# Kernel tuning notes

Hardware: AMD Instinct MI355X
Metric: run time of the kernel (lower is better)

## Reference

```python
import jax, jax.numpy as jnp
from jax import lax
import numpy as np

B, N, C = 8, 4096, 64
NPOINT = 1024
RADII = (0.1, 0.2, 0.4)
NSAMPLES = (16, 32, 128)
MLPS = ((32, 32, 64), (64, 64, 128), (64, 96, 128))


def setup_inputs() -> dict:
    key = jax.random.key(0)
    ks = jax.random.split(key, 32)
    inp = {
        "xyz": jax.random.uniform(ks[0], (B, N, 3), jnp.float32),
        "points": jax.random.normal(ks[1], (B, N, C), jnp.float32),
    }
    k = 2
    for bi, widths in enumerate(MLPS):
        cin = C + 3  # use_xyz concatenates relative coords
        for li, cout in enumerate(widths):
            inp[f"w{bi}_{li}"] = jax.random.normal(ks[k], (cin, cout), jnp.float32) * (1.0 / np.sqrt(cin))
            k += 1
            inp[f"b{bi}_{li}"] = jnp.zeros((cout,), jnp.float32)
            cin = cout
    return inp


def farthest_point_sample(xyz, npoint):
    # xyz: [B,N,3] -> idx [B,npoint] int32. Deterministic start at point 0.
    Bb, Nn, _ = xyz.shape

    def step(carry, _):
        dists, farthest = carry  # [B,N], [B]
        centroid = jnp.take_along_axis(xyz, farthest[:, None, None], axis=1)  # [B,1,3]
        d = jnp.sum((xyz - centroid) ** 2, axis=-1)
        dists = jnp.minimum(dists, d)
        return (dists, jnp.argmax(dists, axis=-1).astype(jnp.int32)), farthest

    init = (jnp.full((Bb, Nn), 1e10, xyz.dtype), jnp.zeros((Bb,), jnp.int32))
    _, idx = lax.scan(step, init, None, length=npoint)
    return jnp.transpose(idx)  # [B, npoint]


def _ball_query(d2, radius, nsample, Nn):
    # d2: [B,S,N] squared distances. First nsample indices (in original order)
    # within radius; empty slots filled with the first valid index (center
    # point is always within its own ball, so a valid index always exists).
    key = jnp.where(d2 < radius * radius, jnp.arange(Nn, dtype=jnp.int32), Nn)
    srt = jnp.sort(key, axis=-1)[..., :nsample]  # [B,S,nsample]
    first = srt[..., :1]
    return jnp.where(srt == Nn, first, srt)


def _group(x, idx):
    # x: [B,N,D], idx: [B,S,K] -> [B,S,K,D]
    return jax.vmap(lambda p, i: p[i])(x, idx)


def _forward(xyz, points, params):
    Nn = xyz.shape[1]
    fps_idx = farthest_point_sample(xyz, NPOINT)                 # [B,S]
    new_xyz = jnp.take_along_axis(xyz, fps_idx[..., None], axis=1)  # [B,S,3]
    d2 = jnp.sum((new_xyz[:, :, None, :] - xyz[:, None, :, :]) ** 2, axis=-1)  # [B,S,N]
    outs = []
    for r, ns, layers in zip(RADII, NSAMPLES, params):
        idx = _ball_query(d2, r, ns, Nn)                          # [B,S,ns]
        g_xyz = _group(xyz, idx) - new_xyz[:, :, None, :]         # [B,S,ns,3]
        g = jnp.concatenate([_group(points, idx), g_xyz], axis=-1)  # [B,S,ns,C+3]
        for w, b in layers:  # 1x1 Conv2d == per-neighbor dense + relu
            g = jax.nn.relu(g @ w + b)
        outs.append(jnp.max(g, axis=2))                           # [B,S,cout]
    return new_xyz, jnp.concatenate(outs, axis=-1)


def reference(xyz, points,
              w0_0, b0_0, w0_1, b0_1, w0_2, b0_2,
              w1_0, b1_0, w1_1, b1_1, w1_2, b1_2,
              w2_0, b2_0, w2_1, b2_1, w2_2, b2_2):
    params = [
        [(w0_0, b0_0), (w0_1, b0_1), (w0_2, b0_2)],
        [(w1_0, b1_0), (w1_1, b1_1), (w1_2, b1_2)],
        [(w2_0, b2_0), (w2_1, b2_1), (w2_2, b2_2)],
    ]
    return _forward(xyz, points, params)
```

## Files before the change

kernel.cpp:

```cpp
#include <hip/hip_runtime.h>
#include <hip/hip_bf16.h>
#include <stdint.h>

typedef unsigned long long u64;
typedef __attribute__((ext_vector_type(8))) short bf16x8;
typedef __attribute__((ext_vector_type(4))) float f32x4;
typedef __attribute__((ext_vector_type(2))) float f32x2;

#define SCOPE_AGENT __HIP_MEMORY_SCOPE_AGENT
#define POISON 0xFFFFFFFFu
#define SPIN_GUARD (1 << 22)

#define H_ITEM 0
#define H_PREP 1
#define H_PLACED 2
#define H_FDONE 3
#define H_SLEEP 4

__device__ __forceinline__ unsigned short f2bf(float f) {
    unsigned x = __float_as_uint(f);
    unsigned r = (x + 0x7fffu + ((x >> 16) & 1u)) >> 16;
    return (unsigned short)r;
}

__device__ __forceinline__ bf16x8 cvt8(float4 a, float4 b) {
    union { bf16x8 v; __hip_bfloat162 h[4]; } u;
    u.h[0] = __float22bfloat162_rn({a.x, a.y});
    u.h[1] = __float22bfloat162_rn({a.z, a.w});
    u.h[2] = __float22bfloat162_rn({b.x, b.y});
    u.h[3] = __float22bfloat162_rn({b.z, b.w});
    return u.v;
}

__device__ __forceinline__ float wave_max_dpp(float v) {
#define DPP_MAX_STEP(ctrl)                                                     \
    v = fmaxf(v, __int_as_float(__builtin_amdgcn_update_dpp(                   \
               0, __float_as_int(v), (ctrl), 0xf, 0xf, true)))
    DPP_MAX_STEP(0xB1);
    DPP_MAX_STEP(0x4E);
    DPP_MAX_STEP(0x141);
    DPP_MAX_STEP(0x140);
    DPP_MAX_STEP(0x142);
    DPP_MAX_STEP(0x143);
#undef DPP_MAX_STEP
    return __int_as_float(__builtin_amdgcn_readlane(__float_as_int(v), 63));
}

__device__ __forceinline__ void lds_barrier() {
    __builtin_amdgcn_sched_barrier(0);
    asm volatile("s_waitcnt lgkmcnt(0)" ::: "memory");
    __builtin_amdgcn_sched_barrier(0);
    __builtin_amdgcn_s_barrier();
    __builtin_amdgcn_sched_barrier(0);
}

__device__ __forceinline__ unsigned cu_key() {
    unsigned hw = (unsigned)__builtin_amdgcn_s_getreg(14852) & 0xffu;
    unsigned xcc = (unsigned)__builtin_amdgcn_s_getreg(6164) & 0x7u;
    return (xcc << 8) | hw;
}

struct WPack { const float* w[9]; const float* b[9]; };

__device__ __forceinline__ void fps_path(const float* __restrict__ xyz,
                                         float* __restrict__ newxyz,
                                         unsigned* __restrict__ hdr,
                                         unsigned* __restrict__ occ,
                                         unsigned char* smem) {
#pragma clang fp contract(off)
    __builtin_amdgcn_s_setprio(3);
    float* xs = (float*)smem;
    float* ys = xs + 4096;
    float* zs = ys + 4096;
    u64* skey = (u64*)(smem + 49152);

    const int b = blockIdx.x;
    const int t = threadIdx.x;
    const int lane = t & 63;
    const int wave = t >> 6;

    if (t == 0) {
        __hip_atomic_store(&occ[cu_key()], 1u, __ATOMIC_RELAXED, SCOPE_AGENT);
        __hip_atomic_fetch_add(&hdr[H_PLACED], 1u, __ATOMIC_RELEASE, SCOPE_AGENT);
    }

    f32x2 px[8], py[8], pz[8], dist[8];
    {
        union { float4 v[12]; float f[48]; } u;
        const float4* src =
            reinterpret_cast<const float4*>(xyz + (size_t)b * 12288) + t * 12;
#pragma unroll
        for (int w = 0; w < 12; ++w) u.v[w] = src[w];
#pragma unroll
        for (int i = 0; i < 8; ++i) {
            px[i] = (f32x2){u.f[6 * i + 0], u.f[6 * i + 3]};
            py[i] = (f32x2){u.f[6 * i + 1], u.f[6 * i + 4]};
            pz[i] = (f32x2){u.f[6 * i + 2], u.f[6 * i + 5]};
            dist[i] = (f32x2){1e10f, 1e10f};
            const int j = t * 16 + 2 * i;
            xs[j] = px[i].x; xs[j + 1] = px[i].y;
            ys[j] = py[i].x; ys[j + 1] = py[i].y;
            zs[j] = pz[i].x; zs[j + 1] = pz[i].y;
        }
    }
    __syncthreads();

    int far = 0;
    for (int k = 0; k < 1024; ++k) {
        const float cx = xs[far], cy = ys[far], cz = zs[far];
        if (t == 0) {
            const size_t o = ((size_t)b * 1024 + k) * 3;
            __hip_atomic_store(&newxyz[o + 0], cx, __ATOMIC_RELAXED, SCOPE_AGENT);
            __hip_atomic_store(&newxyz[o + 1], cy, __ATOMIC_RELAXED, SCOPE_AGENT);
            __hip_atomic_store(&newxyz[o + 2], cz, __ATOMIC_RELAXED, SCOPE_AGENT);
        }
        const f32x2 c2x = (f32x2){cx, cx};
        const f32x2 c2y = (f32x2){cy, cy};
        const f32x2 c2z = (f32x2){cz, cz};
#pragma unroll
        for (int i = 0; i < 8; ++i) {
            const f32x2 dx = px[i] - c2x;
            const f32x2 dy = py[i] - c2y;
            const f32x2 dz = pz[i] - c2z;
            const f32x2 s = dx * dx + dy * dy;
            const f32x2 d = s + dz * dz;
            dist[i].x = fminf(dist[i].x, d.x);
            dist[i].y = fminf(dist[i].y, d.y);
        }
        float dv[16];
#pragma unroll
        for (int i = 0; i < 8; ++i) { dv[2 * i] = dist[i].x; dv[2 * i + 1] = dist[i].y; }
        float m8[8], m4[4], bv;
#pragma unroll
        for (int i = 0; i < 8; ++i) m8[i] = fmaxf(dv[i], dv[i + 8]);
#pragma unroll
        for (int i = 0; i < 4; ++i) m4[i] = fmaxf(m8[i], m8[i + 4]);
        bv = fmaxf(fmaxf(m4[0], m4[1]), fmaxf(m4[2], m4[3]));
        int bj = 15;
#pragma unroll
        for (int i = 14; i >= 0; --i) bj = (dv[i] == bv) ? i : bj;
        const int myidx = t * 16 + bj;

        const float wmax = wave_max_dpp(bv);
        const u64 mask = __ballot(bv == wmax);
        const int fl = (int)__builtin_ctzll(mask);
        const int widx = __builtin_amdgcn_readlane(myidx, fl);

        const int pp = k & 1;
        if (lane == 0)
            skey[pp * 4 + wave] =
                ((u64)__float_as_uint(wmax) << 32) | (unsigned)(4095 - widx);
        lds_barrier();
        const ulonglong2 ka = *reinterpret_cast<const ulonglong2*>(&skey[pp * 4 + 0]);
        const ulonglong2 kb = *reinterpret_cast<const ulonglong2*>(&skey[pp * 4 + 2]);
        const u64 m01 = (ka.x > ka.y) ? ka.x : ka.y;
        const u64 m23 = (kb.x > kb.y) ? kb.x : kb.y;
        const u64 mm = (m01 > m23) ? m01 : m23;
        far = 4095 - (int)(unsigned)(mm & 0xffffffffull);
    }
    if (t == 0)
        __hip_atomic_fetch_add(&hdr[H_FDONE], 1u, __ATOMIC_RELEASE, SCOPE_AGENT);
}

__device__ __forceinline__ void prep_path(const WPack& p,
                                          unsigned short* __restrict__ wout,
                                          float* __restrict__ bout,
                                          unsigned* __restrict__ hdr) {
    constexpr int cin[9]  = {67, 32, 32,  67, 64, 64,  67, 64, 96};
    constexpr int cout[9] = {32, 32, 64,  64, 64, 128, 64, 96, 128};
    constexpr int sw[9]   = {104, 40, 40, 104, 72, 72, 104, 72, 104};
    constexpr int woff[9] = {0, 3328, 4608, 7168, 13824, 18432, 27648, 34304, 41216};
    constexpr int boff[9] = {0, 32, 64, 128, 192, 256, 384, 448, 544};
    const int L = blockIdx.x - 8;
    const float* w = p.w[L];
    const int ci = cin[L], co = cout[L], s = sw[L];
    unsigned short* dst = wout + woff[L];
    for (int e = threadIdx.x; e < co * s; e += 256) {
        const int n = e / s, k = e % s;
        dst[e] = (k < ci) ? f2bf(w[(size_t)k * co + n]) : (unsigned short)0;
    }
    for (int e = threadIdx.x; e < co; e += 256) bout[boff[L] + e] = p.b[L][e];
    __syncthreads();
    if (threadIdx.x == 0)
        __hip_atomic_fetch_add(&hdr[H_PREP], 1u, __ATOMIC_RELEASE, SCOPE_AGENT);
}

__device__ __forceinline__ void poll_centroid(const float* __restrict__ newxyz,
                                              int g, int lane,
                                              float& ncx, float& ncy, float& ncz) {
    const unsigned* ncw = (const unsigned*)(newxyz + (size_t)g * 3);
    unsigned w0 = 0, w1 = 0, w2 = 0;
    if (lane == 0) {
        int n = 0;
        for (;;) {
            w0 = __hip_atomic_load(&ncw[0], __ATOMIC_RELAXED, SCOPE_AGENT);
            w1 = __hip_atomic_load(&ncw[1], __ATOMIC_RELAXED, SCOPE_AGENT);
            w2 = __hip_atomic_load(&ncw[2], __ATOMIC_RELAXED, SCOPE_AGENT);
            if (w0 != POISON && w1 != POISON && w2 != POISON) break;
            if (++n > SPIN_GUARD) break;
            if (n < 64) __builtin_amdgcn_s_sleep(8);
            else        __builtin_amdgcn_s_sleep(32);
        }
    }
    ncx = __uint_as_float((unsigned)__builtin_amdgcn_readfirstlane((int)w0));
    ncy = __uint_as_float((unsigned)__builtin_amdgcn_readfirstlane((int)w1));
    ncz = __uint_as_float((unsigned)__builtin_amdgcn_readfirstlane((int)w2));
}

template <int NS>
__device__ __forceinline__ void ballq1(const float* __restrict__ base,
                                       float cx, float cy, float cz, float r2,
                                       unsigned short* __restrict__ out, int lane) {
    int cnt = 0, first = 0;
    const u64 lower = (((u64)1) << lane) - 1;
    for (int it = 0; it < 64; ++it) {
        const int j = it * 64 + lane;
        const float* pp = base + j * 3;
        const float dx = pp[0] - cx;
        const float dy = pp[1] - cy;
        const float dz = pp[2] - cz;
        const float d2 = __fadd_rn(__fadd_rn(__fmul_rn(dx, dx), __fmul_rn(dy, dy)),
                                   __fmul_rn(dz, dz));
        const bool in = d2 < r2;
        const u64 m = __ballot(in);
        if (cnt == 0 && m) first = it * 64 + (int)__builtin_ctzll(m);
        const int pos = cnt + (int)__builtin_popcountll(m & lower);
        if (in && pos < NS) out[pos] = (unsigned short)j;
        cnt += (int)__builtin_popcountll(m);
        if (cnt >= NS) break;
    }
    for (int pos = cnt + lane; pos < NS; pos += 64) out[pos] = (unsigned short)first;
}

template <int MW, int Cout, int SOUT>
__device__ __forceinline__ void layer1_direct(
    const float* __restrict__ pts,
    const float* __restrict__ xyzb,
    const unsigned short* __restrict__ idxb,
    float ncx, float ncy, float ncz,
    const unsigned short* __restrict__ Wg, const float* __restrict__ bg,
    unsigned short* __restrict__ dst, int lane, int mslice) {
    constexpr int SW = 104;
    constexpr int MT = MW / 16;
    constexpr int NT = Cout / 16;
    const int ml = lane & 15;
    const int quad = lane >> 4;

    bf16x8 afr[MT][3];
#pragma unroll
    for (int mt = 0; mt < MT; ++mt) {
        const int row = mslice * MW + mt * 16 + ml;
        const int id = idxb[row] & 4095;
        const float* rb = pts + ((size_t)id << 6) + quad * 8;
        const float4* r4 = reinterpret_cast<const float4*>(rb);
        afr[mt][0] = cvt8(r4[0], r4[1]);
        const float4* r4b = reinterpret_cast<const float4*>(rb + 32);
        afr[mt][1] = cvt8(r4b[0], r4b[1]);
        union { bf16x8 v; unsigned short h[8]; } tg;
        tg.v = (bf16x8)(short)0;
        if (quad == 0) {
            const float* pz = xyzb + (size_t)id * 3;
            tg.h[0] = f2bf(pz[0] - ncx);
            tg.h[1] = f2bf(pz[1] - ncy);
            tg.h[2] = f2bf(pz[2] - ncz);
        }
        afr[mt][2] = tg.v;
    }

    f32x4 acc[MT][NT];
#pragma unroll
    for (int mt = 0; mt < MT; ++mt)
#pragma unroll
        for (int nt = 0; nt < NT; ++nt) acc[mt][nt] = (f32x4){0.f, 0.f, 0.f, 0.f};

#pragma unroll
    for (int ks = 0; ks < 3; ++ks) {
        bf16x8 bfr[NT];
#pragma unroll
        for (int nt = 0; nt < NT; ++nt)
            bfr[nt] = *reinterpret_cast<const bf16x8*>(
                Wg + (nt * 16 + ml) * SW + ks * 32 + quad * 8);
#pragma unroll
        for (int mt = 0; mt < MT; ++mt)
#pragma unroll
            for (int nt = 0; nt < NT; ++nt)
                acc[mt][nt] = __builtin_amdgcn_mfma_f32_16x16x32_bf16(
                    afr[mt][ks], bfr[nt], acc[mt][nt], 0, 0, 0);
    }

#pragma unroll
    for (int nt = 0; nt < NT; ++nt) {
        const int col = nt * 16 + ml;
        const float bv = bg[col];
#pragma unroll
        for (int mt = 0; mt < MT; ++mt)
#pragma unroll
            for (int r = 0; r < 4; ++r) {
                const float v = fmaxf(acc[mt][nt][r] + bv, 0.0f);
                dst[(mslice * MW + mt * 16 + quad * 4 + r) * SOUT + col] = f2bf(v);
            }
    }
}

template <int MW, int Kp, int Cout, int SIN>
__device__ __forceinline__ void layer_mid(const unsigned short* __restrict__ src,
                                          unsigned short* __restrict__ dst,
                                          const unsigned short* __restrict__ Wg,
                                          const float* __restrict__ bg,
                                          int lane, int mslice) {
    constexpr int MT = MW / 16;
    constexpr int NT = Cout / 16;
    constexpr int SOUT = Cout + 8;
    const int ml = lane & 15;
    const int quad = lane >> 4;

    f32x4 acc[MT][NT];
#pragma unroll
    for (int mt = 0; mt < MT; ++mt)
#pragma unroll
        for (int nt = 0; nt < NT; ++nt) acc[mt][nt] = (f32x4){0.f, 0.f, 0.f, 0.f};

#pragma unroll
    for (int ks = 0; ks < Kp; ks += 32) {
        bf16x8 afr[MT], bfr[NT];
#pragma unroll
        for (int mt = 0; mt < MT; ++mt)
            afr[mt] = *reinterpret_cast<const bf16x8*>(
                src + (mslice * MW + mt * 16 + ml) * SIN + ks + quad * 8);
#pragma unroll
        for (int nt = 0; nt < NT; ++nt)
            bfr[nt] = *reinterpret_cast<const bf16x8*>(
                Wg + (nt * 16 + ml) * SIN + ks + quad * 8);
#pragma unroll
        for (int mt = 0; mt < MT; ++mt)
#pragma unroll
            for (int nt = 0; nt < NT; ++nt)
                acc[mt][nt] = __builtin_amdgcn_mfma_f32_16x16x32_bf16(
                    afr[mt], bfr[nt], acc[mt][nt], 0, 0, 0);
    }

#pragma unroll
    for (int nt = 0; nt < NT; ++nt) {
        const int col = nt * 16 + ml;
        const float bv = bg[col];
#pragma unroll
        for (int mt = 0; mt < MT; ++mt)
#pragma unroll
            for (int r = 0; r < 4; ++r) {
                const float v = fmaxf(acc[mt][nt][r] + bv, 0.0f);
                dst[(mslice * MW + mt * 16 + quad * 4 + r) * SOUT + col] = f2bf(v);
            }
    }
}

template <int MW, int Kp, int Cout, int SIN, bool DIRECT>
__device__ __forceinline__ void layer_last(const unsigned short* __restrict__ src,
                                           const unsigned short* __restrict__ Wg,
                                           const float* __restrict__ bg,
                                           float* __restrict__ out,
                                           int lane, int mslice) {
    constexpr int MT = MW / 16;
    constexpr int NT = Cout / 16;
    const int ml = lane & 15;
    const int quad = lane >> 4;

    f32x4 acc[MT][NT];
#pragma unroll
    for (int mt = 0; mt < MT; ++mt)
#pragma unroll
        for (int nt = 0; nt < NT; ++nt) acc[mt][nt] = (f32x4){0.f, 0.f, 0.f, 0.f};

#pragma unroll
    for (int ks = 0; ks < Kp; ks += 32) {
        bf16x8 afr[MT], bfr[NT];
#pragma unroll
        for (int mt = 0; mt < MT; ++mt)
            afr[mt] = *reinterpret_cast<const bf16x8*>(
                src + (mslice * MW + mt * 16 + ml) * SIN + ks + quad * 8);
#pragma unroll
        for (int nt = 0; nt < NT; ++nt)
            bfr[nt] = *reinterpret_cast<const bf16x8*>(
                Wg + (nt * 16 + ml) * SIN + ks + quad * 8);
#pragma unroll
        for (int mt = 0; mt < MT; ++mt)
#pragma unroll
            for (int nt = 0; nt < NT; ++nt)
                acc[mt][nt] = __builtin_amdgcn_mfma_f32_16x16x32_bf16(
                    afr[mt], bfr[nt], acc[mt][nt], 0, 0, 0);
    }

#pragma unroll
    for (int nt = 0; nt < NT; ++nt) {
        const int col = nt * 16 + ml;
        const float bv = bg[col];
        float mx = 0.0f;
#pragma unroll
        for (int mt = 0; mt < MT; ++mt)
#pragma unroll
            for (int r = 0; r < 4; ++r) mx = fmaxf(mx, acc[mt][nt][r] + bv);
        mx = fmaxf(mx, __shfl_xor(mx, 16, 64));
        mx = fmaxf(mx, __shfl_xor(mx, 32, 64));
        if (quad == 0) {
            if constexpr (DIRECT) out[col] = mx;
            else atomicMax(reinterpret_cast<int*>(out + col), __float_as_int(mx));
        }
    }
}

template <int NS, int C1, int C2, int C3, int CH_OFF>
__device__ __forceinline__ void consume_small(
    unsigned char* smem, const float* __restrict__ xyz,
    const float* __restrict__ points, const float* __restrict__ newxyz,
    const unsigned short* wg1, const unsigned short* wg2, const unsigned short* wg3,
    const float* bg1, const float* bg2, const float* bg3,
    float* __restrict__ outfeat, int gbase, int bb, float r2) {
    constexpr int SB = C1 + 8, SC = C2 + 8;
    unsigned short* Bb = (unsigned short*)smem;
    unsigned short* Cb = Bb + 4 * NS * SB;
    unsigned short* idxb = Cb + 4 * NS * SC;
    const int lane = threadIdx.x & 63;
    const int wave = threadIdx.x >> 6;
    const int g = gbase + wave;
    float ncx, ncy, ncz;
    poll_centroid(newxyz, g, lane, ncx, ncy, ncz);
    const float* xb = xyz + (size_t)bb * 12288;
    unsigned short* idxw = idxb + wave * NS;
    ballq1<NS>(xb, ncx, ncy, ncz, r2, idxw, lane);
    layer1_direct<NS, C1, SB>(points + ((size_t)bb << 18), xb, idxw, ncx, ncy, ncz,
                              wg1, bg1, Bb + wave * NS * SB, lane, 0);
    layer_mid<NS, C1, C2, SB>(Bb + wave * NS * SB, Cb + wave * NS * SC, wg2, bg2,
                              lane, 0);
    layer_last<NS, C2, C3, SC, true>(Cb + wave * NS * SC, wg3, bg3,
                                     outfeat + (size_t)g * 320 + CH_OFF, lane, 0);
}

__device__ __forceinline__ void consume_b3(
    unsigned char* smem, const float* __restrict__ xyz,
    const float* __restrict__ points, const float* __restrict__ newxyz,
    const unsigned short* wg1, const unsigned short* wg2, const unsigned short* wg3,
    const float* bg1, const float* bg2, const float* bg3,
    float* __restrict__ outfeat, int g, int bb) {
    constexpr int SB = 72, SC = 104;
    unsigned short* Bb = (unsigned short*)smem;
    unsigned short* Cb = Bb + 128 * SB;
    float* Mx = (float*)(Cb + 128 * SC);
    unsigned short* idxb = (unsigned short*)(Mx + 128);
    float* mail = (float*)(idxb + 128);
    const int tid = threadIdx.x;
    const int lane = tid & 63;
    const int wave = tid >> 6;
    const float* xb = xyz + (size_t)bb * 12288;
    float ncx, ncy, ncz;
    if (wave == 0) {
        poll_centroid(newxyz, g, lane, ncx, ncy, ncz);
        if (lane == 0) { mail[0] = ncx; mail[1] = ncy; mail[2] = ncz; }
        ballq1<128>(xb, ncx, ncy, ncz, 0.16f, idxb, lane);
    }
    if (tid >= 128) Mx[tid - 128] = 0.0f;
    __syncthreads();
    if (wave != 0) { ncx = mail[0]; ncy = mail[1]; ncz = mail[2]; }
    layer1_direct<32, 64, SB>(points + ((size_t)bb << 18), xb, idxb, ncx, ncy, ncz,
                              wg1, bg1, Bb, lane, wave);
    layer_mid<32, 64, 96, SB>(Bb, Cb, wg2, bg2, lane, wave);
    layer_last<32, 96, 128, SC, false>(Cb, wg3, bg3, Mx, lane, wave);
    __syncthreads();
    if (tid < 128) outfeat[(size_t)g * 320 + 192 + tid] = Mx[tid];
}

__global__ __launch_bounds__(256, 3) void mega_kernel(
    const float* __restrict__ xyz, const float* __restrict__ points, WPack p,
    float* __restrict__ newxyz, float* __restrict__ outfeat,
    unsigned* __restrict__ hdr, unsigned* __restrict__ occ,
    unsigned short* __restrict__ wprep, float* __restrict__ bprep) {
    __shared__ __align__(16) unsigned char smem[49408];
    __shared__ int itemLDS[2];
    const int bx = blockIdx.x;
    if (bx < 8) { fps_path(xyz, newxyz, hdr, occ, smem); return; }
    if (bx < 17) prep_path(p, wprep, bprep, hdr);

    if (threadIdx.x == 0) {
        int n = 0;
        while (__hip_atomic_load(&hdr[H_PLACED], __ATOMIC_RELAXED, SCOPE_AGENT) < 8u &&
               ++n < SPIN_GUARD)
            __builtin_amdgcn_s_sleep(2);
        (void)__hip_atomic_load(&hdr[H_PLACED], __ATOMIC_ACQUIRE, SCOPE_AGENT);
        bool doze = (bx >= 17) && ((bx & 255) < 8);
        if (!doze &&
            __hip_atomic_load(&occ[cu_key()], __ATOMIC_RELAXED, SCOPE_AGENT)) {
            const unsigned prev = __hip_atomic_fetch_add(&hdr[H_SLEEP], 1u,
                                                         __ATOMIC_RELAXED, SCOPE_AGENT);
            doze = (prev < 24u);
        }
        n = 0;
        if (doze)
            while (__hip_atomic_load(&hdr[H_FDONE], __ATOMIC_RELAXED, SCOPE_AGENT) < 8u &&
                   ++n < SPIN_GUARD)
                __builtin_amdgcn_s_sleep(127);
        n = 0;
        while (__hip_atomic_load(&hdr[H_PREP], __ATOMIC_RELAXED, SCOPE_AGENT) < 9u &&
               ++n < SPIN_GUARD)
            __builtin_amdgcn_s_sleep(8);
        (void)__hip_atomic_load(&hdr[H_PREP], __ATOMIC_ACQUIRE, SCOPE_AGENT);
    }

    for (int slot = 0;; slot ^= 1) {
        if (threadIdx.x == 0)
            itemLDS[slot] = (int)__hip_atomic_fetch_add(&hdr[H_ITEM], 1u,
                                                        __ATOMIC_RELAXED, SCOPE_AGENT);
        __syncthreads();
        const int item = itemLDS[slot];
        if (item >= 12288) break;

        const int chunk = item / 48;
        const int r = item - chunk * 48;
        int bb, br, soff = 0;
        if (r < 8)       { br = 0; bb = r; }
        else if (r < 16) { br = 1; bb = r - 8; }
        else             { br = 2; bb = (r - 16) & 7; soff = (r - 16) >> 3; }
        const int gbase = bb * 1024 + chunk * 4;
        if (br == 0)
            consume_small<16, 32, 32, 64, 0>(smem, xyz, points, newxyz,
                wprep + 0, wprep + 3328, wprep + 4608,
                bprep + 0, bprep + 32, bprep + 64, outfeat, gbase, bb, 0.01f);
        else if (br == 1)
            consume_small<32, 64, 64, 128, 64>(smem, xyz, points, newxyz,
                wprep + 7168, wprep + 13824, wprep + 18432,
                bprep + 128, bprep + 192, bprep + 256, outfeat, gbase, bb, 0.04f);
        else
            consume_b3(smem, xyz, points, newxyz,
                wprep + 27648, wprep + 34304, wprep + 41216,
                bprep + 384, bprep + 448, bprep + 544, outfeat, gbase + soff, bb);
    }
}

extern "C" void kernel_launch(void* const* d_in, const int* in_sizes, int n_in,
                              void* d_out, int out_size, void* d_ws, size_t ws_size,
                              hipStream_t stream) {
    (void)in_sizes; (void)n_in; (void)out_size; (void)ws_size;
    const float* xyz = (const float*)d_in[0];
    const float* points = (const float*)d_in[1];
    WPack pack;
    int p = 2;
    for (int L = 0; L < 9; ++L) {
        pack.w[L] = (const float*)d_in[p++];
        pack.b[L] = (const float*)d_in[p++];
    }
    float* newxyz = (float*)d_out;
    float* outfeat = (float*)d_out + 8 * 1024 * 3;

    unsigned* hdr = (unsigned*)d_ws;
    unsigned* occ = (unsigned*)((char*)d_ws + 256);
    unsigned short* wprep = (unsigned short*)((char*)d_ws + 8448);
    float* bprep = (float*)((char*)d_ws + 8448 + 109056);

    (void)hipMemsetAsync(d_ws, 0, 8448, stream);
    (void)hipMemsetAsync(newxyz, 0xFF, 8 * 1024 * 3 * 4, stream);
    mega_kernel<<<dim3(768), dim3(256), 0, stream>>>(
        xyz, points, pack, newxyz, outfeat, hdr, occ, wprep, bprep);
}
```

Baseline: 644.9 us.

## Double block size to 512 threads, spreading FPS and group work over eight waves

The persistent mega-kernel moves from 768 blocks of 256 threads to 512 blocks of 512 threads. Each FPS block now holds 8 points per thread and reduces across 8 waves instead of 4. The grouping consumers handle 8 groups per work unit (two batches by four centroids), and branch 3 splits its per-group MLP over 16 rows per wave. This aims to shorten the serial FPS loop per iteration and amortise work-item fetching, at the cost of more LDS per block, fewer co-resident blocks, and a wider barrier in the FPS loop.

```diff
diff --git a/kernel.cpp b/kernel.cpp
--- a/kernel.cpp
+++ b/kernel.cpp
@@ -84,20 +84,20 @@
         __hip_atomic_fetch_add(&hdr[H_PLACED], 1u, __ATOMIC_RELEASE, SCOPE_AGENT);
     }
 
-    f32x2 px[8], py[8], pz[8], dist[8];
+    f32x2 px[4], py[4], pz[4], dist[4];
     {
-        union { float4 v[12]; float f[48]; } u;
+        union { float4 v[6]; float f[24]; } u;
         const float4* src =
-            reinterpret_cast<const float4*>(xyz + (size_t)b * 12288) + t * 12;
-#pragma unroll
-        for (int w = 0; w < 12; ++w) u.v[w] = src[w];
-#pragma unroll
-        for (int i = 0; i < 8; ++i) {
+            reinterpret_cast<const float4*>(xyz + (size_t)b * 12288) + t * 6;
+#pragma unroll
+        for (int w = 0; w < 6; ++w) u.v[w] = src[w];
+#pragma unroll
+        for (int i = 0; i < 4; ++i) {
             px[i] = (f32x2){u.f[6 * i + 0], u.f[6 * i + 3]};
             py[i] = (f32x2){u.f[6 * i + 1], u.f[6 * i + 4]};
             pz[i] = (f32x2){u.f[6 * i + 2], u.f[6 * i + 5]};
             dist[i] = (f32x2){1e10f, 1e10f};
-            const int j = t * 16 + 2 * i;
+            const int j = t * 8 + 2 * i;
             xs[j] = px[i].x; xs[j + 1] = px[i].y;
             ys[j] = py[i].x; ys[j + 1] = py[i].y;
             zs[j] = pz[i].x; zs[j + 1] = pz[i].y;
@@ -118,7 +118,7 @@
         const f32x2 c2y = (f32x2){cy, cy};
         const f32x2 c2z = (f32x2){cz, cz};
 #pragma unroll
-        for (int i = 0; i < 8; ++i) {
+        for (int i = 0; i < 4; ++i) {
             const f32x2 dx = px[i] - c2x;
             const f32x2 dy = py[i] - c2y;
             const f32x2 dz = pz[i] - c2z;
@@ -127,19 +127,17 @@
             dist[i].x = fminf(dist[i].x, d.x);
             dist[i].y = fminf(dist[i].y, d.y);
         }
-        float dv[16];
-#pragma unroll
-        for (int i = 0; i < 8; ++i) { dv[2 * i] = dist[i].x; dv[2 * i + 1] = dist[i].y; }
-        float m8[8], m4[4], bv;
-#pragma unroll
-        for (int i = 0; i < 8; ++i) m8[i] = fmaxf(dv[i], dv[i + 8]);
-#pragma unroll
-        for (int i = 0; i < 4; ++i) m4[i] = fmaxf(m8[i], m8[i + 4]);
+        float dv[8];
+#pragma unroll
+        for (int i = 0; i < 4; ++i) { dv[2 * i] = dist[i].x; dv[2 * i + 1] = dist[i].y; }
+        float m4[4], bv;
+#pragma unroll
+        for (int i = 0; i < 4; ++i) m4[i] = fmaxf(dv[i], dv[i + 4]);
         bv = fmaxf(fmaxf(m4[0], m4[1]), fmaxf(m4[2], m4[3]));
-        int bj = 15;
-#pragma unroll
-        for (int i = 14; i >= 0; --i) bj = (dv[i] == bv) ? i : bj;
-        const int myidx = t * 16 + bj;
+        int bj = 7;
+#pragma unroll
+        for (int i = 6; i >= 0; --i) bj = (dv[i] == bv) ? i : bj;
+        const int myidx = t * 8 + bj;
 
         const float wmax = wave_max_dpp(bv);
         const u64 mask = __ballot(bv == wmax);
@@ -148,14 +146,20 @@
 
         const int pp = k & 1;
         if (lane == 0)
-            skey[pp * 4 + wave] =
+            skey[pp * 8 + wave] =
                 ((u64)__float_as_uint(wmax) << 32) | (unsigned)(4095 - widx);
         lds_barrier();
-        const ulonglong2 ka = *reinterpret_cast<const ulonglong2*>(&skey[pp * 4 + 0]);
-        const ulonglong2 kb = *reinterpret_cast<const ulonglong2*>(&skey[pp * 4 + 2]);
+        const ulonglong2 ka = *reinterpret_cast<const ulonglong2*>(&skey[pp * 8 + 0]);
+        const ulonglong2 kb = *reinterpret_cast<const ulonglong2*>(&skey[pp * 8 + 2]);
+        const ulonglong2 kc = *reinterpret_cast<const ulonglong2*>(&skey[pp * 8 + 4]);
+        const ulonglong2 kd = *reinterpret_cast<const ulonglong2*>(&skey[pp * 8 + 6]);
         const u64 m01 = (ka.x > ka.y) ? ka.x : ka.y;
         const u64 m23 = (kb.x > kb.y) ? kb.x : kb.y;
-        const u64 mm = (m01 > m23) ? m01 : m23;
+        const u64 m45 = (kc.x > kc.y) ? kc.x : kc.y;
+        const u64 m67 = (kd.x > kd.y) ? kd.x : kd.y;
+        const u64 ma = (m01 > m23) ? m01 : m23;
+        const u64 mb = (m45 > m67) ? m45 : m67;
+        const u64 mm = (ma > mb) ? ma : mb;
         far = 4095 - (int)(unsigned)(mm & 0xffffffffull);
     }
     if (t == 0)
@@ -175,11 +179,11 @@
     const float* w = p.w[L];
     const int ci = cin[L], co = cout[L], s = sw[L];
     unsigned short* dst = wout + woff[L];
-    for (int e = threadIdx.x; e < co * s; e += 256) {
+    for (int e = threadIdx.x; e < co * s; e += 512) {
         const int n = e / s, k = e % s;
         dst[e] = (k < ci) ? f2bf(w[(size_t)k * co + n]) : (unsigned short)0;
     }
-    for (int e = threadIdx.x; e < co; e += 256) bout[boff[L] + e] = p.b[L][e];
+    for (int e = threadIdx.x; e < co; e += 512) bout[boff[L] + e] = p.b[L][e];
     __syncthreads();
     if (threadIdx.x == 0)
         __hip_atomic_fetch_add(&hdr[H_PREP], 1u, __ATOMIC_RELEASE, SCOPE_AGENT);
@@ -413,14 +417,13 @@
     const float* __restrict__ points, const float* __restrict__ newxyz,
     const unsigned short* wg1, const unsigned short* wg2, const unsigned short* wg3,
     const float* bg1, const float* bg2, const float* bg3,
-    float* __restrict__ outfeat, int gbase, int bb, float r2) {
+    float* __restrict__ outfeat, int g, int bb, float r2) {
     constexpr int SB = C1 + 8, SC = C2 + 8;
     unsigned short* Bb = (unsigned short*)smem;
-    unsigned short* Cb = Bb + 4 * NS * SB;
-    unsigned short* idxb = Cb + 4 * NS * SC;
+    unsigned short* Cb = Bb + 8 * NS * SB;
+    unsigned short* idxb = Cb + 8 * NS * SC;
     const int lane = threadIdx.x & 63;
     const int wave = threadIdx.x >> 6;
-    const int g = gbase + wave;
     float ncx, ncy, ncz;
     poll_centroid(newxyz, g, lane, ncx, ncy, ncz);
     const float* xb = xyz + (size_t)bb * 12288;
@@ -456,23 +459,23 @@
         if (lane == 0) { mail[0] = ncx; mail[1] = ncy; mail[2] = ncz; }
         ballq1<128>(xb, ncx, ncy, ncz, 0.16f, idxb, lane);
     }
-    if (tid >= 128) Mx[tid - 128] = 0.0f;
+    if (tid >= 128 && tid < 256) Mx[tid - 128] = 0.0f;
     __syncthreads();
     if (wave != 0) { ncx = mail[0]; ncy = mail[1]; ncz = mail[2]; }
-    layer1_direct<32, 64, SB>(points + ((size_t)bb << 18), xb, idxb, ncx, ncy, ncz,
+    layer1_direct<16, 64, SB>(points + ((size_t)bb << 18), xb, idxb, ncx, ncy, ncz,
                               wg1, bg1, Bb, lane, wave);
-    layer_mid<32, 64, 96, SB>(Bb, Cb, wg2, bg2, lane, wave);
-    layer_last<32, 96, 128, SC, false>(Cb, wg3, bg3, Mx, lane, wave);
+    layer_mid<16, 64, 96, SB>(Bb, Cb, wg2, bg2, lane, wave);
+    layer_last<16, 96, 128, SC, false>(Cb, wg3, bg3, Mx, lane, wave);
     __syncthreads();
     if (tid < 128) outfeat[(size_t)g * 320 + 192 + tid] = Mx[tid];
 }
 
-__global__ __launch_bounds__(256, 3) void mega_kernel(
+__global__ __launch_bounds__(512, 4) void mega_kernel(
     const float* __restrict__ xyz, const float* __restrict__ points, WPack p,
     float* __restrict__ newxyz, float* __restrict__ outfeat,
     unsigned* __restrict__ hdr, unsigned* __restrict__ occ,
     unsigned short* __restrict__ wprep, float* __restrict__ bprep) {
-    __shared__ __align__(16) unsigned char smem[49408];
+    __shared__ __align__(16) unsigned char smem[74240];
     __shared__ int itemLDS[2];
     const int bx = blockIdx.x;
     if (bx < 8) { fps_path(xyz, newxyz, hdr, occ, smem); return; }
@@ -489,7 +492,7 @@
             __hip_atomic_load(&occ[cu_key()], __ATOMIC_RELAXED, SCOPE_AGENT)) {
             const unsigned prev = __hip_atomic_fetch_add(&hdr[H_SLEEP], 1u,
                                                          __ATOMIC_RELAXED, SCOPE_AGENT);
-            doze = (prev < 24u);
+            doze = (prev < 16u);
         }
         n = 0;
         if (doze)
@@ -503,33 +506,37 @@
         (void)__hip_atomic_load(&hdr[H_PREP], __ATOMIC_ACQUIRE, SCOPE_AGENT);
     }
 
+    const int wave = threadIdx.x >> 6;
     for (int slot = 0;; slot ^= 1) {
         if (threadIdx.x == 0)
             itemLDS[slot] = (int)__hip_atomic_fetch_add(&hdr[H_ITEM], 1u,
                                                         __ATOMIC_RELAXED, SCOPE_AGENT);
         __syncthreads();
-        const int item = itemLDS[slot];
-        if (item >= 12288) break;
-
-        const int chunk = item / 48;
-        const int r = item - chunk * 48;
-        int bb, br, soff = 0;
-        if (r < 8)       { br = 0; bb = r; }
-        else if (r < 16) { br = 1; bb = r - 8; }
-        else             { br = 2; bb = (r - 16) & 7; soff = (r - 16) >> 3; }
-        const int gbase = bb * 1024 + chunk * 4;
-        if (br == 0)
+        const int unit = itemLDS[slot];
+        if (unit >= 10240) break;
+
+        const int chunk = unit / 40;
+        const int r = unit - chunk * 40;
+        if (r < 4) {
+            const int bb = 2 * r + (wave >> 2);
+            const int g = bb * 1024 + chunk * 4 + (wave & 3);
             consume_small<16, 32, 32, 64, 0>(smem, xyz, points, newxyz,
                 wprep + 0, wprep + 3328, wprep + 4608,
-                bprep + 0, bprep + 32, bprep + 64, outfeat, gbase, bb, 0.01f);
-        else if (br == 1)
+                bprep + 0, bprep + 32, bprep + 64, outfeat, g, bb, 0.01f);
+        } else if (r < 8) {
+            const int bb = 2 * (r - 4) + (wave >> 2);
+            const int g = bb * 1024 + chunk * 4 + (wave & 3);
             consume_small<32, 64, 64, 128, 64>(smem, xyz, points, newxyz,
                 wprep + 7168, wprep + 13824, wprep + 18432,
-                bprep + 128, bprep + 192, bprep + 256, outfeat, gbase, bb, 0.04f);
-        else
+                bprep + 128, bprep + 192, bprep + 256, outfeat, g, bb, 0.04f);
+        } else {
+            const int q = r - 8;
+            const int bb = q & 7;
+            const int g = bb * 1024 + chunk * 4 + (q >> 3);
             consume_b3(smem, xyz, points, newxyz,
                 wprep + 27648, wprep + 34304, wprep + 41216,
-                bprep + 384, bprep + 448, bprep + 544, outfeat, gbase + soff, bb);
+                bprep + 384, bprep + 448, bprep + 544, outfeat, g, bb);
+        }
     }
 }
 
@@ -555,6 +562,6 @@
 
     (void)hipMemsetAsync(d_ws, 0, 8448, stream);
     (void)hipMemsetAsync(newxyz, 0xFF, 8 * 1024 * 3 * 4, stream);
-    mega_kernel<<<dim3(768), dim3(256), 0, stream>>>(
+    mega_kernel<<<dim3(512), dim3(512), 0, stream>>>(
         xyz, points, pack, newxyz, outfeat, hdr, occ, wprep, bprep);
 }
```

Measured after the change: 863.9 us. +33.9%, slower.
